# Kernel tuning notes

Measured on AMD Instinct MI355X. Metric: run time of the kernel, lower is better.

Reference implementation:

```python
import jax, jax.numpy as jnp
import numpy as np

N = 100000      # nodes
E = 500000      # edges
NODE_IN = 60
EDGE_IN = 8
H = 256         # hidden
L = 8           # GINEConv layers
G = 64          # graphs in batch
BN_EPS = 1e-5


def setup_inputs() -> dict:
    key = jax.random.key(0)
    ks = jax.random.split(key, 40)
    s = 0.05
    f32 = jnp.float32
    inp = {
        "x": jax.random.normal(ks[0], (N, NODE_IN), f32),
        "edge_index": jax.random.randint(ks[1], (2, E), 0, N),
        "edge_attr": jax.random.normal(ks[2], (E, EDGE_IN), f32),
        "batch": jnp.sort(jax.random.randint(ks[3], (N,), 0, G)),
        # x_proj: Linear(node_in->H) + BatchNorm1d (eval-mode running stats)
        "xproj_W": jax.random.normal(ks[4], (NODE_IN, H), f32) * s,
        "xproj_b": jnp.zeros((H,), f32),
        "xp_gamma": jnp.ones((H,), f32),
        "xp_beta": jnp.zeros((H,), f32),
        "xp_mean": jax.random.normal(ks[5], (H,), f32) * 0.01,
        "xp_var": jax.random.uniform(ks[6], (H,), f32, 0.5, 1.5),
        # stacked GINEConv params (L layers)
        "edge_W": jax.random.normal(ks[7], (L, EDGE_IN, H), f32) * s,
        "edge_b": jnp.zeros((L, H), f32),
        "mlp_W1": jax.random.normal(ks[8], (L, H, H), f32) * s,
        "mlp_b1": jnp.zeros((L, H), f32),
        "mlp_W2": jax.random.normal(ks[9], (L, H, H), f32) * s,
        "mlp_b2": jnp.zeros((L, H), f32),
        "eps": jnp.zeros((L,), f32),  # GINE eps (default 0, not trained)
        # per-layer BatchNorm (eval-mode)
        "bn_gamma": jnp.ones((L, H), f32),
        "bn_beta": jnp.zeros((L, H), f32),
        "bn_mean": jax.random.normal(ks[10], (L, H), f32) * 0.01,
        "bn_var": jax.random.uniform(ks[11], (L, H), f32, 0.5, 1.5),
        # head: Linear(H->H/2) ReLU Dropout Linear(H/2->1)
        "head_W1": jax.random.normal(ks[12], (H, H // 2), f32) * s,
        "head_b1": jnp.zeros((H // 2,), f32),
        "head_W2": jax.random.normal(ks[13], (H // 2, 1), f32) * s,
        "head_b2": jnp.zeros((1,), f32),
    }
    return inp


def _bn(x, gamma, beta, mean, var):
    # eval-mode BatchNorm1d with running stats
    return (x - mean) * (gamma * jax.lax.rsqrt(var + BN_EPS)) + beta


def reference(x, edge_index, edge_attr, batch,
              xproj_W, xproj_b, xp_gamma, xp_beta, xp_mean, xp_var,
              edge_W, edge_b, mlp_W1, mlp_b1, mlp_W2, mlp_b2, eps,
              bn_gamma, bn_beta, bn_mean, bn_var,
              head_W1, head_b1, head_W2, head_b2):
    src, dst = edge_index[0], edge_index[1]  # source -> target aggregation
    # x_proj: Linear + BN + ReLU
    h = jax.nn.relu(_bn(x @ xproj_W + xproj_b, xp_gamma, xp_beta, xp_mean, xp_var))
    for l in range(L):
        # GINEConv: msg = ReLU(x_j + lin(edge_attr)); sum-aggregate at target
        e = edge_attr @ edge_W[l] + edge_b[l]                 # [E,H]
        m = jax.nn.relu(h[src] + e)                           # [E,H] gather + add
        agg = jax.ops.segment_sum(m, dst, num_segments=N)     # [N,H] scatter-add
        z = (1.0 + eps[l]) * h + agg
        z = jax.nn.relu(z @ mlp_W1[l] + mlp_b1[l]) @ mlp_W2[l] + mlp_b2[l]
        # BN + ReLU (dropout is identity in eval)
        h = jax.nn.relu(_bn(z, bn_gamma[l], bn_beta[l], bn_mean[l], bn_var[l]))
    # global_mean_pool over batch ids
    gsum = jax.ops.segment_sum(h, batch, num_segments=G)      # [G,H]
    cnt = jax.ops.segment_sum(jnp.ones((N, 1), h.dtype), batch, num_segments=G)
    g = gsum / jnp.maximum(cnt, 1.0)
    # head MLP -> scalar per graph
    hid = jax.nn.relu(g @ head_W1 + head_b1)
    out = (hid @ head_W2 + head_b2)[:, 0]                     # [G]
    return out
```

## Files before the change

kernel.cpp:

```cpp
#include <hip/hip_runtime.h>

#define N_NODES 100000
#define N_EDGES 500000
#define NODE_IN 60
#define EDGE_IN 8
#define HID 256
#define NLAYERS 8
#define NGRAPH 64
#define BN_EPS 1e-5f
#define SY_PITCH 520

typedef __attribute__((ext_vector_type(4))) float f32x4;
typedef __attribute__((ext_vector_type(4))) short short4v;
typedef __attribute__((ext_vector_type(8))) short short8v;
typedef __attribute__((ext_vector_type(4))) unsigned short u16x4;
typedef unsigned short u16;

__device__ __forceinline__ u16 f2bf(float f) {
    unsigned int u = __builtin_bit_cast(unsigned int, f);
    u += 0x7fffu + ((u >> 16) & 1u);
    return (u16)(u >> 16);
}
__device__ __forceinline__ float bf2f(u16 u) {
    unsigned int x = ((unsigned int)u) << 16;
    return __builtin_bit_cast(float, x);
}
__device__ __forceinline__ float lo_f(unsigned int d) {
    return __builtin_bit_cast(float, d << 16);
}
__device__ __forceinline__ float hi_f(unsigned int d) {
    return __builtin_bit_cast(float, d & 0xffff0000u);
}

__device__ __forceinline__ void g2lds16(const void* g, void* l) {
    __builtin_amdgcn_global_load_lds(
        (const __attribute__((address_space(1))) void*)g,
        (__attribute__((address_space(3))) void*)l, 16, 0, 0);
}

template<int KT, bool WITH_BN>
__global__ __launch_bounds__(256, 2)
void mfma_gemm(const u16* A, const u16* Bt,
               const float* __restrict__ bias,
               const float* __restrict__ gamma, const float* __restrict__ beta,
               const float* __restrict__ mean,  const float* __restrict__ var,
               u16* Cout, int M)
{
    __shared__ u16 smem[24576];
    u16* sA = smem;
    u16* sB = smem + 8192;

    const int tid  = threadIdx.x;
    const int lane = tid & 63;
    const int wv   = tid >> 6;
    const int lrow = lane & 15;
    const int g    = lane >> 4;
    const int m0   = blockIdx.x * 128;
    const int ldab = KT * 128;
    const int lsub = lane >> 3;
    const int gsw  = ((lane & 7) * 16) ^ (lsub << 4);

    f32x4 acc[8][4] = {};

    for (int kt = 0; kt < KT; ++kt) {
        #pragma unroll
        for (int i = 0; i < 4; ++i) {
            const int row = i * 32 + wv * 8 + lsub;
            g2lds16((const char*)A + (size_t)(m0 + row) * ldab + kt * 128 + gsw,
                    (char*)sA + i * 4096 + wv * 1024);
        }
        #pragma unroll
        for (int i = 0; i < 8; ++i) {
            const int row = i * 32 + wv * 8 + lsub;
            g2lds16((const char*)Bt + (size_t)row * ldab + kt * 128 + gsw,
                    (char*)sB + i * 4096 + wv * 1024);
        }
        __syncthreads();

        #pragma unroll
        for (int ks = 0; ks < 2; ++ks) {
            const int off1 = ks * 64 + 8 * g;
            const int off2 = off1 + 32;
            short8v bfrag[4];
            #pragma unroll
            for (int nb = 0; nb < 4; ++nb) {
                const int col = wv * 64 + nb * 16 + lrow;
                const int sw  = (col & 7) << 4;
                short4v lo = *(const short4v*)((const char*)sB + col * 128 + (off1 ^ sw));
                short4v hi = *(const short4v*)((const char*)sB + col * 128 + (off2 ^ sw));
                short8v b;
                b[0] = lo[0]; b[1] = lo[1]; b[2] = lo[2]; b[3] = lo[3];
                b[4] = hi[0]; b[5] = hi[1]; b[6] = hi[2]; b[7] = hi[3];
                bfrag[nb] = b;
            }
            #pragma unroll
            for (int mb = 0; mb < 8; ++mb) {
                const int row = mb * 16 + lrow;
                const int sw  = (row & 7) << 4;
                short4v lo = *(const short4v*)((const char*)sA + row * 128 + (off1 ^ sw));
                short4v hi = *(const short4v*)((const char*)sA + row * 128 + (off2 ^ sw));
                short8v a;
                a[0] = lo[0]; a[1] = lo[1]; a[2] = lo[2]; a[3] = lo[3];
                a[4] = hi[0]; a[5] = hi[1]; a[6] = hi[2]; a[7] = hi[3];
                #pragma unroll
                for (int nb = 0; nb < 4; ++nb)
                    acc[mb][nb] = __builtin_amdgcn_mfma_f32_16x16x32_bf16(a, bfrag[nb], acc[mb][nb], 0, 0, 0);
            }
        }
        __syncthreads();
    }

    #pragma unroll
    for (int mb = 0; mb < 8; ++mb) {
        #pragma unroll
        for (int r = 0; r < 4; ++r) {
            const int row = m0 + mb * 16 + g * 4 + r;
            if (row >= M) continue;
            #pragma unroll
            for (int nb = 0; nb < 4; ++nb) {
                const int col = wv * 64 + nb * 16 + lrow;
                float v = acc[mb][nb][r] + bias[col];
                if constexpr (WITH_BN)
                    v = (v - mean[col]) * (gamma[col] * rsqrtf(var[col] + BN_EPS)) + beta[col];
                v = fmaxf(v, 0.f);
                Cout[(size_t)row * HID + col] = f2bf(v);
            }
        }
    }
}

__global__ __launch_bounds__(256, 3)
void fused_mlp(const u16* __restrict__ Z, const u16* __restrict__ W1p,
               const u16* __restrict__ W2p,
               const float* __restrict__ b1,
               const float* __restrict__ scale2, const float* __restrict__ shift2,
               u16* __restrict__ Hout, int M)
{
    __shared__ u16 smem[16640];
    u16* sZ = smem;
    u16* sY = smem;

    const int tid  = threadIdx.x;
    const int lane = tid & 63;
    const int wv   = tid >> 6;
    const int lrow = lane & 15;
    const int g    = lane >> 4;
    const int m0   = blockIdx.x * 64;
    const int lsub = lane >> 3;
    const int gsw  = ((lane & 7) * 16) ^ (lsub << 4);

    #pragma unroll
    for (int kt = 0; kt < 4; ++kt) {
        #pragma unroll
        for (int i = 0; i < 2; ++i) {
            const int row = i * 32 + wv * 8 + lsub;
            g2lds16((const char*)Z + (size_t)(m0 + row) * 512 + kt * 128 + gsw,
                    (char*)sZ + kt * 8192 + i * 4096 + wv * 1024);
        }
    }
    __syncthreads();

    f32x4 acc[4][4] = {};
    #pragma unroll
    for (int kt = 0; kt < 4; ++kt) {
        #pragma unroll
        for (int ks = 0; ks < 2; ++ks) {
            const int off1 = ks * 64 + 8 * g;
            const int off2 = off1 + 32;
            short8v bfrag[4];
            #pragma unroll
            for (int nb = 0; nb < 4; ++nb) {
                const int cb = wv * 4 + nb;
                u16x4 lo = *(const u16x4*)&W1p[((((kt * 2 + ks) * 2 + 0) * 16 + cb) << 8) + lane * 4];
                u16x4 hi = *(const u16x4*)&W1p[((((kt * 2 + ks) * 2 + 1) * 16 + cb) << 8) + lane * 4];
                short8v b;
                b[0] = (short)lo[0]; b[1] = (short)lo[1]; b[2] = (short)lo[2]; b[3] = (short)lo[3];
                b[4] = (short)hi[0]; b[5] = (short)hi[1]; b[6] = (short)hi[2]; b[7] = (short)hi[3];
                bfrag[nb] = b;
            }
            #pragma unroll
            for (int mb = 0; mb < 4; ++mb) {
                const int row = mb * 16 + lrow;
                const int sw  = (row & 7) << 4;
                short4v lo = *(const short4v*)((const char*)sZ + kt * 8192 + row * 128 + (off1 ^ sw));
                short4v hi = *(const short4v*)((const char*)sZ + kt * 8192 + row * 128 + (off2 ^ sw));
                short8v a;
                a[0] = lo[0]; a[1] = lo[1]; a[2] = lo[2]; a[3] = lo[3];
                a[4] = hi[0]; a[5] = hi[1]; a[6] = hi[2]; a[7] = hi[3];
                #pragma unroll
                for (int nb = 0; nb < 4; ++nb)
                    acc[mb][nb] = __builtin_amdgcn_mfma_f32_16x16x32_bf16(a, bfrag[nb], acc[mb][nb], 0, 0, 0);
            }
        }
    }
    __syncthreads();

    float b1v[4];
    #pragma unroll
    for (int nb = 0; nb < 4; ++nb) b1v[nb] = b1[wv * 64 + nb * 16 + lrow];
    #pragma unroll
    for (int mb = 0; mb < 4; ++mb) {
        #pragma unroll
        for (int r = 0; r < 4; ++r) {
            const int row = mb * 16 + g * 4 + r;
            #pragma unroll
            for (int nb = 0; nb < 4; ++nb) {
                const int col = wv * 64 + nb * 16 + lrow;
                const float v = fmaxf(acc[mb][nb][r] + b1v[nb], 0.f);
                *(u16*)((char*)sY + row * SY_PITCH + col * 2) = f2bf(v);
            }
        }
    }
    __syncthreads();

    f32x4 acc2[4][4] = {};
    #pragma unroll
    for (int kt2 = 0; kt2 < 4; ++kt2) {
        #pragma unroll
        for (int ks = 0; ks < 2; ++ks) {
            const int off1 = ks * 64 + 8 * g;
            const int yo1  = kt2 * 128 + off1;
            const int yo2  = yo1 + 32;
            short8v bfrag[4];
            #pragma unroll
            for (int nb = 0; nb < 4; ++nb) {
                const int cb = wv * 4 + nb;
                u16x4 lo = *(const u16x4*)&W2p[((((kt2 * 2 + ks) * 2 + 0) * 16 + cb) << 8) + lane * 4];
                u16x4 hi = *(const u16x4*)&W2p[((((kt2 * 2 + ks) * 2 + 1) * 16 + cb) << 8) + lane * 4];
                short8v b;
                b[0] = (short)lo[0]; b[1] = (short)lo[1]; b[2] = (short)lo[2]; b[3] = (short)lo[3];
                b[4] = (short)hi[0]; b[5] = (short)hi[1]; b[6] = (short)hi[2]; b[7] = (short)hi[3];
                bfrag[nb] = b;
            }
            #pragma unroll
            for (int mb = 0; mb < 4; ++mb) {
                const int row = mb * 16 + lrow;
                short4v lo = *(const short4v*)((const char*)sY + row * SY_PITCH + yo1);
                short4v hi = *(const short4v*)((const char*)sY + row * SY_PITCH + yo2);
                short8v a;
                a[0] = lo[0]; a[1] = lo[1]; a[2] = lo[2]; a[3] = lo[3];
                a[4] = hi[0]; a[5] = hi[1]; a[6] = hi[2]; a[7] = hi[3];
                #pragma unroll
                for (int nb = 0; nb < 4; ++nb)
                    acc2[mb][nb] = __builtin_amdgcn_mfma_f32_16x16x32_bf16(a, bfrag[nb], acc2[mb][nb], 0, 0, 0);
            }
        }
    }

    float scl[4], shf[4];
    #pragma unroll
    for (int nb = 0; nb < 4; ++nb) {
        const int col = wv * 64 + nb * 16 + lrow;
        scl[nb] = scale2[col];
        shf[nb] = shift2[col];
    }
    #pragma unroll
    for (int mb = 0; mb < 4; ++mb) {
        #pragma unroll
        for (int r = 0; r < 4; ++r) {
            const int row = m0 + mb * 16 + g * 4 + r;
            if (row >= M) continue;
            #pragma unroll
            for (int nb = 0; nb < 4; ++nb) {
                const int col = wv * 64 + nb * 16 + lrow;
                const float v = fmaxf(acc2[mb][nb][r] * scl[nb] + shf[nb], 0.f);
                Hout[(size_t)row * HID + col] = f2bf(v);
            }
        }
    }
}

__global__ __launch_bounds__(256)
void convw_kernel(const float* __restrict__ W, u16* __restrict__ Wp)
{
    size_t i = (size_t)blockIdx.x * 256 + threadIdx.x;
    const int mat  = (int)(i >> 16);
    const int r    = (int)(i & 65535);
    const int j    = r & 3;
    const int lane = (r >> 2) & 63;
    const int cb   = (r >> 8) & 15;
    const int half = (r >> 12) & 1;
    const int ks   = (r >> 13) & 1;
    const int kt   = (r >> 14) & 3;
    const int col = cb * 16 + (lane & 15);
    const int k   = kt * 64 + ks * 32 + 4 * (lane >> 4) + 16 * half + j;
    Wp[i] = f2bf(W[(size_t)mat * 65536 + (size_t)k * 256 + col]);
}

__global__ __launch_bounds__(256)
void convwx_kernel(const float* __restrict__ W, u16* __restrict__ Wt)
{
    int i = blockIdx.x * 256 + threadIdx.x;
    const int n = i >> 6, k = i & 63;
    Wt[i] = (k < NODE_IN) ? f2bf(W[(size_t)k * HID + n]) : (u16)0;
}

__global__ __launch_bounds__(256)
void convx_kernel(const float* __restrict__ x, u16* __restrict__ xbf)
{
    size_t i = (size_t)blockIdx.x * 256 + threadIdx.x;
    if (i >= (size_t)N_NODES * 64) return;
    const int n = (int)(i >> 6), k = (int)(i & 63);
    xbf[i] = (k < NODE_IN) ? f2bf(x[(size_t)n * NODE_IN + k]) : (u16)0;
}

__global__ __launch_bounds__(256)
void bnfold_kernel(const float* __restrict__ b2, const float* __restrict__ gamma,
                   const float* __restrict__ beta, const float* __restrict__ mean,
                   const float* __restrict__ var,
                   float* __restrict__ scale, float* __restrict__ shift)
{
    int i = blockIdx.x * 256 + threadIdx.x;
    if (i >= NLAYERS * HID) return;
    const float s = gamma[i] * rsqrtf(var[i] + BN_EPS);
    scale[i] = s;
    shift[i] = (b2[i] - mean[i]) * s + beta[i];
}

__global__ __launch_bounds__(256)
void deg_count_kernel(const int* __restrict__ dst, int* __restrict__ deg, int E)
{
    int e = blockIdx.x * 256 + threadIdx.x;
    if (e < E) atomicAdd(&deg[dst[e]], 1);
}

__global__ __launch_bounds__(256)
void scan1_kernel(const int* __restrict__ deg, int* __restrict__ rowptr,
                  int* __restrict__ bsum, int n)
{
    __shared__ int s[256];
    const int tid = threadIdx.x;
    const int i = blockIdx.x * 256 + tid;
    const int v = (i < n) ? deg[i] : 0;
    s[tid] = v;
    __syncthreads();
    #pragma unroll
    for (int d = 1; d < 256; d <<= 1) {
        int t = (tid >= d) ? s[tid - d] : 0;
        __syncthreads();
        s[tid] += t;
        __syncthreads();
    }
    if (i < n) rowptr[i] = s[tid] - v;
    if (tid == 255) bsum[blockIdx.x] = s[255];
}

__global__ void scan2_kernel(int* bsum, int nb, int* rowptr, int n)
{
    if (threadIdx.x == 0 && blockIdx.x == 0) {
        int run = 0;
        for (int j = 0; j < nb; ++j) { int t = bsum[j]; bsum[j] = run; run += t; }
        rowptr[n] = run;
    }
}

__global__ __launch_bounds__(256)
void scan3_kernel(int* __restrict__ rowptr, const int* __restrict__ bsum, int n)
{
    int i = blockIdx.x * 256 + threadIdx.x;
    if (i < n) rowptr[i] += bsum[i >> 8];
}

__global__ __launch_bounds__(256)
void scatter_kernel(const int* __restrict__ src, const int* __restrict__ dst,
                    const float* __restrict__ ea,
                    const int* __restrict__ rowptr, int* __restrict__ fill,
                    int* __restrict__ esrc, u16* __restrict__ eap, int E)
{
    int e = blockIdx.x * 256 + threadIdx.x;
    if (e >= E) return;
    const int d = dst[e];
    const int pos = rowptr[d] + atomicAdd(&fill[d], 1);
    esrc[pos] = src[e];
    const float4 a0 = *(const float4*)&ea[(size_t)e * EDGE_IN];
    const float4 a1 = *(const float4*)&ea[(size_t)e * EDGE_IN + 4];
    u16x4 p0, p1;
    p0[0] = f2bf(a0.x); p0[1] = f2bf(a0.y); p0[2] = f2bf(a0.z); p0[3] = f2bf(a0.w);
    p1[0] = f2bf(a1.x); p1[1] = f2bf(a1.y); p1[2] = f2bf(a1.z); p1[3] = f2bf(a1.w);
    *(u16x4*)&eap[(size_t)pos * EDGE_IN]     = p0;
    *(u16x4*)&eap[(size_t)pos * EDGE_IN + 4] = p1;
}

__global__ __launch_bounds__(256, 8)
void agg_kernel(const u16* __restrict__ h, const u16* __restrict__ eap,
                const int* __restrict__ rowptr, const int* __restrict__ esrc,
                const float* __restrict__ W, const float* __restrict__ b,
                const float* __restrict__ eps, int l, u16* __restrict__ z)
{
    const int lane  = threadIdx.x & 63;
    const int wv    = threadIdx.x >> 6;
    const int c0    = lane * 4;
    const int lofsB = lane * 8;

    f32x4 Wr[EDGE_IN];
    #pragma unroll
    for (int k = 0; k < EDGE_IN; ++k) Wr[k] = *(const f32x4*)&W[k * HID + c0];
    const f32x4 br = *(const f32x4*)&b[c0];
    const float e1 = 1.0f + eps[l];

    for (int n = blockIdx.x * 4 + wv; n < N_NODES; n += gridDim.x * 4) {
        const int beg = __builtin_amdgcn_readfirstlane(rowptr[n]);
        const int end = __builtin_amdgcn_readfirstlane(rowptr[n + 1]);
        const int end1 = end - 1;

        const u16x4 hv = *(const u16x4*)&h[(size_t)n * HID + c0];
        float a0 = e1 * bf2f(hv[0]), a1 = e1 * bf2f(hv[1]);
        float a2 = e1 * bf2f(hv[2]), a3 = e1 * bf2f(hv[3]);

        for (int i0 = beg; i0 < end; i0 += 4) {
            int idx0 = i0;
            int idx1 = (i0 + 1 < end) ? i0 + 1 : end1;
            int idx2 = (i0 + 2 < end) ? i0 + 2 : end1;
            int idx3 = (i0 + 3 < end) ? i0 + 3 : end1;

            const int sb0 = __builtin_amdgcn_readfirstlane(esrc[idx0]) << 9;
            const int sb1 = __builtin_amdgcn_readfirstlane(esrc[idx1]) << 9;
            const int sb2 = __builtin_amdgcn_readfirstlane(esrc[idx2]) << 9;
            const int sb3 = __builtin_amdgcn_readfirstlane(esrc[idx3]) << 9;

            u16x4 hs0 = *(const u16x4*)((const char*)h + (unsigned)(sb0 + lofsB));
            u16x4 hs1 = *(const u16x4*)((const char*)h + (unsigned)(sb1 + lofsB));
            u16x4 hs2 = *(const u16x4*)((const char*)h + (unsigned)(sb2 + lofsB));
            u16x4 hs3 = *(const u16x4*)((const char*)h + (unsigned)(sb3 + lofsB));

            uint4 t0 = *(const uint4*)&eap[(size_t)idx0 * EDGE_IN];
            uint4 t1 = *(const uint4*)&eap[(size_t)idx1 * EDGE_IN];
            uint4 t2 = *(const uint4*)&eap[(size_t)idx2 * EDGE_IN];
            uint4 t3 = *(const uint4*)&eap[(size_t)idx3 * EDGE_IN];

            #pragma unroll
            for (int j = 0; j < 4; ++j) {
                if (i0 + j < end) {
                    const uint4 tt = (j == 0) ? t0 : (j == 1) ? t1 : (j == 2) ? t2 : t3;
                    const u16x4 hh = (j == 0) ? hs0 : (j == 1) ? hs1 : (j == 2) ? hs2 : hs3;
                    const unsigned dx = __builtin_amdgcn_readfirstlane((int)tt.x);
                    const unsigned dy = __builtin_amdgcn_readfirstlane((int)tt.y);
                    const unsigned dz = __builtin_amdgcn_readfirstlane((int)tt.z);
                    const unsigned dw = __builtin_amdgcn_readfirstlane((int)tt.w);
                    f32x4 ev = br;
                    ev += lo_f(dx) * Wr[0];
                    ev += hi_f(dx) * Wr[1];
                    ev += lo_f(dy) * Wr[2];
                    ev += hi_f(dy) * Wr[3];
                    ev += lo_f(dz) * Wr[4];
                    ev += hi_f(dz) * Wr[5];
                    ev += lo_f(dw) * Wr[6];
                    ev += hi_f(dw) * Wr[7];
                    a0 += fmaxf(bf2f(hh[0]) + ev[0], 0.f);
                    a1 += fmaxf(bf2f(hh[1]) + ev[1], 0.f);
                    a2 += fmaxf(bf2f(hh[2]) + ev[2], 0.f);
                    a3 += fmaxf(bf2f(hh[3]) + ev[3], 0.f);
                }
            }
        }
        u16x4 o;
        o[0] = f2bf(a0); o[1] = f2bf(a1); o[2] = f2bf(a2); o[3] = f2bf(a3);
        *(u16x4*)&z[(size_t)n * HID + c0] = o;
    }
}

__global__ __launch_bounds__(256)
void pool_kernel(const u16* __restrict__ h, const int* __restrict__ batch,
                 float* __restrict__ gsum, int* __restrict__ cnt, int n)
{
    const int lane = threadIdx.x & 63;
    const int wv   = threadIdx.x >> 6;
    const int c0   = lane * 4;
    const int n0   = blockIdx.x * 64;

    f32x4 acc = {0.f, 0.f, 0.f, 0.f};
    int gcur = -1;
    int c = 0;

    for (int i = wv; i < 64; i += 4) {
        const int node = n0 + i;
        if (node >= n) break;
        const int g = __builtin_amdgcn_readfirstlane(batch[node]);
        if (g != gcur) {
            if (gcur >= 0) {
                atomicAdd(&gsum[gcur * HID + c0 + 0], acc[0]);
                atomicAdd(&gsum[gcur * HID + c0 + 1], acc[1]);
                atomicAdd(&gsum[gcur * HID + c0 + 2], acc[2]);
                atomicAdd(&gsum[gcur * HID + c0 + 3], acc[3]);
                if (lane == 0) atomicAdd(&cnt[gcur], c);
            }
            acc = (f32x4){0.f, 0.f, 0.f, 0.f};
            c = 0;
            gcur = g;
        }
        const u16x4 hv = *(const u16x4*)&h[(size_t)node * HID + c0];
        acc[0] += bf2f(hv[0]);
        acc[1] += bf2f(hv[1]);
        acc[2] += bf2f(hv[2]);
        acc[3] += bf2f(hv[3]);
        c++;
    }
    if (gcur >= 0) {
        atomicAdd(&gsum[gcur * HID + c0 + 0], acc[0]);
        atomicAdd(&gsum[gcur * HID + c0 + 1], acc[1]);
        atomicAdd(&gsum[gcur * HID + c0 + 2], acc[2]);
        atomicAdd(&gsum[gcur * HID + c0 + 3], acc[3]);
        if (lane == 0) atomicAdd(&cnt[gcur], c);
    }
}

__global__ __launch_bounds__(128)
void head_kernel(const float* __restrict__ gsum, const int* __restrict__ cnt,
                 const float* __restrict__ W1, const float* __restrict__ b1,
                 const float* __restrict__ W2, const float* __restrict__ b2,
                 float* __restrict__ out)
{
    const int gi = blockIdx.x;
    const int j = threadIdx.x;
    __shared__ float gs[HID];
    __shared__ float red[128];

    const float c = fmaxf((float)cnt[gi], 1.0f);
    gs[j]       = gsum[gi * HID + j] / c;
    gs[j + 128] = gsum[gi * HID + 128 + j] / c;
    __syncthreads();

    float acc = b1[j];
    #pragma unroll 8
    for (int k = 0; k < HID; ++k) acc += gs[k] * W1[k * 128 + j];
    acc = fmaxf(acc, 0.f);
    red[j] = acc * W2[j];
    __syncthreads();
    for (int s = 64; s > 0; s >>= 1) {
        if (j < s) red[j] += red[j + s];
        __syncthreads();
    }
    if (j == 0) out[gi] = red[0] + b2[0];
}

extern "C" void kernel_launch(void* const* d_in, const int* in_sizes, int n_in,
                              void* d_out, int out_size, void* d_ws, size_t ws_size,
                              hipStream_t stream)
{
    const float* x         = (const float*)d_in[0];
    const int*   ei        = (const int*)d_in[1];
    const float* edge_attr = (const float*)d_in[2];
    const int*   batch     = (const int*)d_in[3];
    const float* xproj_W   = (const float*)d_in[4];
    const float* xproj_b   = (const float*)d_in[5];
    const float* xp_gamma  = (const float*)d_in[6];
    const float* xp_beta   = (const float*)d_in[7];
    const float* xp_mean   = (const float*)d_in[8];
    const float* xp_var    = (const float*)d_in[9];
    const float* edge_W    = (const float*)d_in[10];
    const float* edge_b    = (const float*)d_in[11];
    const float* mlp_W1    = (const float*)d_in[12];
    const float* mlp_b1    = (const float*)d_in[13];
    const float* mlp_W2    = (const float*)d_in[14];
    const float* mlp_b2    = (const float*)d_in[15];
    const float* eps       = (const float*)d_in[16];
    const float* bn_gamma  = (const float*)d_in[17];
    const float* bn_beta   = (const float*)d_in[18];
    const float* bn_mean   = (const float*)d_in[19];
    const float* bn_var    = (const float*)d_in[20];
    const float* head_W1   = (const float*)d_in[21];
    const float* head_b1   = (const float*)d_in[22];
    const float* head_W2   = (const float*)d_in[23];
    const float* head_b2   = (const float*)d_in[24];
    float* out = (float*)d_out;

    const int* srcI = ei;
    const int* dstI = ei + N_EDGES;

    char* w = (char*)d_ws;
    u16*   h      = (u16*)w;                 w += (size_t)N_NODES * HID * 2;
    u16*   zy     = (u16*)w;                 w += (size_t)N_NODES * HID * 2;
    u16*   xbf    = (u16*)w;                 w += (size_t)N_NODES * 64 * 2;
    u16*   Wp1    = (u16*)w;                 w += (size_t)NLAYERS * 65536 * 2;
    u16*   Wp2    = (u16*)w;                 w += (size_t)NLAYERS * 65536 * 2;
    u16*   Wxt    = (u16*)w;                 w += 16384 * 2;
    float* scale2 = (float*)w;               w += NLAYERS * HID * 4;
    float* shift2 = (float*)w;               w += NLAYERS * HID * 4;
    int*   rowptr = (int*)w;                 w += 100032 * 4;
    int*   deg    = (int*)w;                 w += 100032 * 4;
    int*   fill   = (int*)w;                 w += 100032 * 4;
    int*   bsum   = (int*)w;                 w += 512 * 4;
    int*   esrc   = (int*)w;                 w += (size_t)N_EDGES * 4;
    u16*   eap    = (u16*)w;                 w += (size_t)N_EDGES * EDGE_IN * 2;
    float* gsum   = (float*)w;               w += NGRAPH * HID * 4;
    int*   cnt    = (int*)w;                 w += NGRAPH * 4;

    convw_kernel<<<2048, 256, 0, stream>>>(mlp_W1, Wp1);
    convw_kernel<<<2048, 256, 0, stream>>>(mlp_W2, Wp2);
    convwx_kernel<<<64, 256, 0, stream>>>(xproj_W, Wxt);
    convx_kernel<<<25000, 256, 0, stream>>>(x, xbf);
    bnfold_kernel<<<8, 256, 0, stream>>>(mlp_b2, bn_gamma, bn_beta, bn_mean, bn_var,
                                         scale2, shift2);

    hipMemsetAsync(deg, 0, 2 * 100032 * sizeof(int), stream);
    deg_count_kernel<<<(N_EDGES + 255) / 256, 256, 0, stream>>>(dstI, deg, N_EDGES);
    scan1_kernel<<<391, 256, 0, stream>>>(deg, rowptr, bsum, N_NODES);
    scan2_kernel<<<1, 64, 0, stream>>>(bsum, 391, rowptr, N_NODES);
    scan3_kernel<<<391, 256, 0, stream>>>(rowptr, bsum, N_NODES);
    scatter_kernel<<<(N_EDGES + 255) / 256, 256, 0, stream>>>(
        srcI, dstI, edge_attr, rowptr, fill, esrc, eap, N_EDGES);

    mfma_gemm<1, true><<<(N_NODES + 127) / 128, 256, 0, stream>>>(
        xbf, Wxt, xproj_b, xp_gamma, xp_beta, xp_mean, xp_var, h, N_NODES);

    const int fgrid = (N_NODES + 63) / 64;
    for (int l = 0; l < NLAYERS; ++l) {
        agg_kernel<<<2048, 256, 0, stream>>>(
            h, eap, rowptr, esrc,
            edge_W + (size_t)l * EDGE_IN * HID, edge_b + (size_t)l * HID,
            eps, l, zy);
        fused_mlp<<<fgrid, 256, 0, stream>>>(
            zy, Wp1 + (size_t)l * 65536, Wp2 + (size_t)l * 65536,
            mlp_b1 + (size_t)l * HID, scale2 + (size_t)l * HID, shift2 + (size_t)l * HID,
            h, N_NODES);
    }

    hipMemsetAsync(gsum, 0, (NGRAPH * HID + NGRAPH) * sizeof(float), stream);
    pool_kernel<<<(N_NODES + 63) / 64, 256, 0, stream>>>(h, batch, gsum, cnt, N_NODES);
    head_kernel<<<NGRAPH, 128, 0, stream>>>(gsum, cnt, head_W1, head_b1, head_W2, head_b2, out);
}
```

Measured before the change: 1.064 ms.

## Double fused MLP row tile to 128 with 8 waves and swizzled intermediate

Each fused_mlp block now handles 128 rows with 512 threads arranged as a 2x4 grid of waves, so every W1/W2 fragment load from global memory serves twice as many rows. The hidden intermediate is written back into the same XOR-swizzled LDS layout as the input tile, replacing the padded-pitch buffer, and LDS per block grows to 64KB. This cuts weight traffic per row and may reduce LDS bank conflicts. The cost is fewer resident blocks per CU and fewer blocks in the grid, and rows past M still read zy out of bounds unless that buffer is padded.

```diff
diff --git a/kernel.cpp b/kernel.cpp
--- a/kernel.cpp
+++ b/kernel.cpp
@@ -8,7 +8,6 @@
 #define NLAYERS 8
 #define NGRAPH 64
 #define BN_EPS 1e-5f
-#define SY_PITCH 520
 
 typedef __attribute__((ext_vector_type(4))) float f32x4;
 typedef __attribute__((ext_vector_type(4))) short short4v;
@@ -129,23 +128,24 @@
     }
 }
 
-__global__ __launch_bounds__(256, 3)
+__global__ __launch_bounds__(512, 4)
 void fused_mlp(const u16* __restrict__ Z, const u16* __restrict__ W1p,
                const u16* __restrict__ W2p,
                const float* __restrict__ b1,
                const float* __restrict__ scale2, const float* __restrict__ shift2,
                u16* __restrict__ Hout, int M)
 {
-    __shared__ u16 smem[16640];
-    u16* sZ = smem;
-    u16* sY = smem;
+    __shared__ u16 smem[32768];
+    u16* zbuf = smem;
 
     const int tid  = threadIdx.x;
     const int lane = tid & 63;
-    const int wv   = tid >> 6;
+    const int w    = tid >> 6;
+    const int wr   = w >> 2;
+    const int wc   = w & 3;
     const int lrow = lane & 15;
     const int g    = lane >> 4;
-    const int m0   = blockIdx.x * 64;
+    const int m0   = blockIdx.x * 128;
     const int lsub = lane >> 3;
     const int gsw  = ((lane & 7) * 16) ^ (lsub << 4);
 
@@ -153,9 +153,9 @@
     for (int kt = 0; kt < 4; ++kt) {
         #pragma unroll
         for (int i = 0; i < 2; ++i) {
-            const int row = i * 32 + wv * 8 + lsub;
+            const int row = i * 64 + w * 8 + lsub;
             g2lds16((const char*)Z + (size_t)(m0 + row) * 512 + kt * 128 + gsw,
-                    (char*)sZ + kt * 8192 + i * 4096 + wv * 1024);
+                    (char*)zbuf + kt * 16384 + i * 8192 + w * 1024);
         }
     }
     __syncthreads();
@@ -170,7 +170,7 @@
             short8v bfrag[4];
             #pragma unroll
             for (int nb = 0; nb < 4; ++nb) {
-                const int cb = wv * 4 + nb;
+                const int cb = wc * 4 + nb;
                 u16x4 lo = *(const u16x4*)&W1p[((((kt * 2 + ks) * 2 + 0) * 16 + cb) << 8) + lane * 4];
                 u16x4 hi = *(const u16x4*)&W1p[((((kt * 2 + ks) * 2 + 1) * 16 + cb) << 8) + lane * 4];
                 short8v b;
@@ -180,10 +180,10 @@
             }
             #pragma unroll
             for (int mb = 0; mb < 4; ++mb) {
-                const int row = mb * 16 + lrow;
+                const int row = wr * 64 + mb * 16 + lrow;
                 const int sw  = (row & 7) << 4;
-                short4v lo = *(const short4v*)((const char*)sZ + kt * 8192 + row * 128 + (off1 ^ sw));
-                short4v hi = *(const short4v*)((const char*)sZ + kt * 8192 + row * 128 + (off2 ^ sw));
+                short4v lo = *(const short4v*)((const char*)zbuf + kt * 16384 + row * 128 + (off1 ^ sw));
+                short4v hi = *(const short4v*)((const char*)zbuf + kt * 16384 + row * 128 + (off2 ^ sw));
                 short8v a;
                 a[0] = lo[0]; a[1] = lo[1]; a[2] = lo[2]; a[3] = lo[3];
                 a[4] = hi[0]; a[5] = hi[1]; a[6] = hi[2]; a[7] = hi[3];
@@ -197,17 +197,19 @@
 
     float b1v[4];
     #pragma unroll
-    for (int nb = 0; nb < 4; ++nb) b1v[nb] = b1[wv * 64 + nb * 16 + lrow];
+    for (int nb = 0; nb < 4; ++nb) b1v[nb] = b1[wc * 64 + nb * 16 + lrow];
     #pragma unroll
     for (int mb = 0; mb < 4; ++mb) {
         #pragma unroll
         for (int r = 0; r < 4; ++r) {
-            const int row = mb * 16 + g * 4 + r;
+            const int row = wr * 64 + mb * 16 + g * 4 + r;
+            const int sw  = (row & 7) << 4;
             #pragma unroll
             for (int nb = 0; nb < 4; ++nb) {
-                const int col = wv * 64 + nb * 16 + lrow;
+                const int col = wc * 64 + nb * 16 + lrow;
                 const float v = fmaxf(acc[mb][nb][r] + b1v[nb], 0.f);
-                *(u16*)((char*)sY + row * SY_PITCH + col * 2) = f2bf(v);
+                *(u16*)((char*)zbuf + (col >> 6) * 16384 + row * 128 +
+                        (((col & 63) * 2) ^ sw)) = f2bf(v);
             }
         }
     }
@@ -219,12 +221,11 @@
         #pragma unroll
         for (int ks = 0; ks < 2; ++ks) {
             const int off1 = ks * 64 + 8 * g;
-            const int yo1  = kt2 * 128 + off1;
-            const int yo2  = yo1 + 32;
+            const int off2 = off1 + 32;
             short8v bfrag[4];
             #pragma unroll
             for (int nb = 0; nb < 4; ++nb) {
-                const int cb = wv * 4 + nb;
+                const int cb = wc * 4 + nb;
                 u16x4 lo = *(const u16x4*)&W2p[((((kt2 * 2 + ks) * 2 + 0) * 16 + cb) << 8) + lane * 4];
                 u16x4 hi = *(const u16x4*)&W2p[((((kt2 * 2 + ks) * 2 + 1) * 16 + cb) << 8) + lane * 4];
                 short8v b;
@@ -234,9 +235,10 @@
             }
             #pragma unroll
             for (int mb = 0; mb < 4; ++mb) {
-                const int row = mb * 16 + lrow;
-                short4v lo = *(const short4v*)((const char*)sY + row * SY_PITCH + yo1);
-                short4v hi = *(const short4v*)((const char*)sY + row * SY_PITCH + yo2);
+                const int row = wr * 64 + mb * 16 + lrow;
+                const int sw  = (row & 7) << 4;
+                short4v lo = *(const short4v*)((const char*)zbuf + kt2 * 16384 + row * 128 + (off1 ^ sw));
+                short4v hi = *(const short4v*)((const char*)zbuf + kt2 * 16384 + row * 128 + (off2 ^ sw));
                 short8v a;
                 a[0] = lo[0]; a[1] = lo[1]; a[2] = lo[2]; a[3] = lo[3];
                 a[4] = hi[0]; a[5] = hi[1]; a[6] = hi[2]; a[7] = hi[3];
@@ -250,7 +252,7 @@
     float scl[4], shf[4];
     #pragma unroll
     for (int nb = 0; nb < 4; ++nb) {
-        const int col = wv * 64 + nb * 16 + lrow;
+        const int col = wc * 64 + nb * 16 + lrow;
         scl[nb] = scale2[col];
         shf[nb] = shift2[col];
     }
@@ -258,11 +260,11 @@
     for (int mb = 0; mb < 4; ++mb) {
         #pragma unroll
         for (int r = 0; r < 4; ++r) {
-            const int row = m0 + mb * 16 + g * 4 + r;
+            const int row = m0 + wr * 64 + mb * 16 + g * 4 + r;
             if (row >= M) continue;
             #pragma unroll
             for (int nb = 0; nb < 4; ++nb) {
-                const int col = wv * 64 + nb * 16 + lrow;
+                const int col = wc * 64 + nb * 16 + lrow;
                 const float v = fmaxf(acc2[mb][nb][r] * scl[nb] + shf[nb], 0.f);
                 Hout[(size_t)row * HID + col] = f2bf(v);
             }
@@ -603,13 +605,13 @@
     mfma_gemm<1, true><<<(N_NODES + 127) / 128, 256, 0, stream>>>(
         xbf, Wxt, xproj_b, xp_gamma, xp_beta, xp_mean, xp_var, h, N_NODES);
 
-    const int fgrid = (N_NODES + 63) / 64;
+    const int fgrid = (N_NODES + 127) / 128;
     for (int l = 0; l < NLAYERS; ++l) {
         agg_kernel<<<2048, 256, 0, stream>>>(
             h, eap, rowptr, esrc,
             edge_W + (size_t)l * EDGE_IN * HID, edge_b + (size_t)l * HID,
             eps, l, zy);
-        fused_mlp<<<fgrid, 256, 0, stream>>>(
+        fused_mlp<<<fgrid, 512, 0, stream>>>(
             zy, Wp1 + (size_t)l * 65536, Wp2 + (size_t)l * 65536,
             mlp_b1 + (size_t)l * HID, scale2 + (size_t)l * HID, shift2 + (size_t)l * HID,
             h, N_NODES);
```

New measurement: 1.210 ms. +13.7%, slower.
